# Kernel optimization log

Hardware: AMD Instinct MI355X
Metric: run time of the kernel (lower is better)

Reference implementation:

```python
import jax, jax.numpy as jnp
import numpy as np

B, L, NT = 4, 512, 20
H, DK, DM = 6, 10, 60  # heads, d_k, d_model (=embedding_dim+1)
ED = 59


def setup_inputs() -> dict:
    key = jax.random.key(0)
    ks = jax.random.split(key, 12)
    # event_seqs[..., 0] = event times (increasing), event_seqs[..., 1] = event type id stored as float
    times = jnp.cumsum(jax.random.uniform(ks[0], (B, L + 1)), axis=1)
    types = jax.random.randint(ks[1], (B, L + 1), 0, NT).astype(jnp.float32)
    event_seqs = jnp.stack([times, types], axis=-1)  # [B, L+1, 2]
    # causal (subsequent) mask, no padding -> lower-triangular [B, L, L]
    src_mask = jnp.broadcast_to(jnp.tril(jnp.ones((L, L), dtype=bool)), (B, L, L))
    w = lambda k, s: jax.random.normal(k, s, dtype=jnp.float32) * 0.1
    return dict(
        event_seqs=event_seqs, src_mask=src_mask,
        embed_w=w(ks[2], (ED, NT)),
        q_w=w(ks[3], (DM, DM)), q_b=jnp.zeros((DM,), jnp.float32),
        k_w=w(ks[4], (DM, DM)), k_b=jnp.zeros((DM,), jnp.float32),
        v_w=w(ks[5], (DM, DM)), v_b=jnp.zeros((DM,), jnp.float32),
        alpha_w=w(ks[6], (DK, DK * H // 2)), alpha_b=jnp.zeros((DK,), jnp.float32),
        gamma_w=w(ks[7], (DK, DK * H // 2)), gamma_b=jnp.zeros((DK,), jnp.float32),
        mu_w=w(ks[8], (DK, DM)), mu_b=jnp.zeros((DK,), jnp.float32),
    )


def reference(event_seqs, src_mask, embed_w, q_w, q_b, k_w, k_b, v_w, v_b,
              alpha_w, alpha_b, gamma_w, gamma_b, mu_w, mu_b):
    b = event_seqs.shape[0]
    # temporal feature: dt between consecutive events (ts padded with leading 0)
    ts = jnp.pad(event_seqs[:, :, 0], ((0, 0), (1, 0)))  # [B, T+1]
    dt = ts[:, 1:] - ts[:, :-1]                           # [B, T]
    temp_feat = dt[:, :-1, None]                          # [B, L, 1]
    types = event_seqs[:, :-1, 1].astype(jnp.int32)       # [B, L]
    type_feat = jax.nn.one_hot(types, NT, dtype=jnp.float32) @ embed_w.T  # [B, L, ED]
    feat = jnp.concatenate([temp_feat, type_feat], axis=-1)  # [B, L, DM]

    def heads(x, w, bias):
        return (x @ w.T + bias).reshape(b, L, H, DK).transpose(0, 2, 1, 3)  # [B,H,L,DK]

    q = heads(feat, q_w, q_b)
    k = heads(feat, k_w, k_b)
    v = heads(feat, v_w, v_b)

    mask4 = src_mask[:, None, :, :]  # [B,1,L,L]
    scores = jnp.einsum('bhid,bhjd->bhij', q, k) / np.sqrt(DK).astype(np.float32)
    scores = jnp.where(mask4, scores, -1e9)
    p_attn = jax.nn.softmax(scores, axis=-1)
    p_attn = jnp.where(mask4, p_attn, 0.0)               # [B,H,L,L]
    v_mu_pre = jnp.einsum('bhij,bhjd->bhid', p_attn, v)  # [B,H,L,DK]

    # per-pair attn * value, split heads in half (faithful to torch view semantics)
    prod = p_attn[..., None] * v[:, :, None, :, :]       # [B,H,L,L,DK]
    hh = H // 2
    x_alpha = prod[:, :hh].reshape(b, L, L, hh * DK)     # raw C-order reshape == torch .view
    x_gamma = prod[:, hh:].reshape(b, L, L, hh * DK)

    v_alpha = jax.nn.softplus(x_alpha @ alpha_w.T + alpha_b)          # Softplus(beta=1)
    v_gamma = jax.nn.softplus(10.0 * (x_gamma @ gamma_w.T + gamma_b)) / 10.0  # Softplus(beta=10)
    pair_mask = src_mask[..., None]                      # [B,L,L,1]
    v_alpha = jnp.where(pair_mask, v_alpha, 0.0)
    v_gamma = jnp.where(pair_mask, v_gamma, 0.0)

    v_mu = jax.nn.sigmoid(v_mu_pre.transpose(0, 2, 1, 3).reshape(b, L, DM) @ mu_w.T + mu_b)  # [B,L,DK]
    return (v_mu, v_alpha, v_gamma)
```

## Files before the change

### kernel.cpp

```cpp
#include <hip/hip_runtime.h>
#include <hip/hip_bf16.h>

#define BB 4
#define LL 512
#define NTYPES 20
#define HH 6
#define DKK 10
#define DMM 60
#define PROW 516
#define NWROW 516

__device__ __forceinline__ float softplus_fast(float x) {
    return fmaxf(x, 0.0f) + __logf(1.0f + __expf(-fabsf(x)));
}

__global__ void ishp_qkv(const float* __restrict__ ev,
                         const float* __restrict__ embed_w,
                         const float* __restrict__ qw, const float* __restrict__ qb,
                         const float* __restrict__ kw, const float* __restrict__ kb,
                         const float* __restrict__ vw, const float* __restrict__ vb,
                         const float* __restrict__ aw, const float* __restrict__ gw,
                         float* __restrict__ q, float* __restrict__ kT, float* __restrict__ vT,
                         float* __restrict__ Wbuf)
{
    int pos = blockIdx.x;
    int b = pos >> 9, l = pos & 511;
    __shared__ float feat[DMM];
    __shared__ float sv[DMM];
    int t = threadIdx.x;
    if (t == 0) {
        float t1 = ev[(b * (LL + 1) + l) * 2 + 0];
        float t0 = (l > 0) ? ev[(b * (LL + 1) + l - 1) * 2 + 0] : 0.0f;
        feat[0] = t1 - t0;
    } else if (t < DMM) {
        int type = (int)ev[(b * (LL + 1) + l) * 2 + 1];
        feat[t] = embed_w[(t - 1) * NTYPES + type];
    }
    __syncthreads();
    if (t < 3 * DMM) {
        int which = t / DMM;
        int m = t - which * DMM;
        const float* w  = which == 0 ? qw : which == 1 ? kw : vw;
        const float* bs = which == 0 ? qb : which == 1 ? kb : vb;
        float s = bs[m];
        #pragma unroll
        for (int c = 0; c < DMM; ++c) s += feat[c] * w[m * DMM + c];
        int h = m / DKK, d = m - h * DKK;
        if (which == 0)      q [((b * HH + h) * LL + l) * DKK + d] = s;
        else if (which == 1) kT[((b * HH + h) * DKK + d) * LL + l] = s;
        else {
            vT[((b * HH + h) * DKK + d) * LL + l] = s;
            sv[m] = s;
        }
    }
    __syncthreads();
    if (t < 180) {
        int kk = t % 10;
        int u = t / 10;
        int h  = u % 3;
        int cc = (u / 3) % 3;
        int mat = u / 9;
        const float* w = mat ? gw : aw;
        float s = 0.0f;
        #pragma unroll
        for (int d = 0; d < DKK; ++d) s += w[kk * 30 + cc * 10 + d] * sv[(h + 3 * mat) * DKK + d];
        int slot = (l % 3) * 172 + l / 3;
        Wbuf[((size_t)((((mat * 3 + cc) * 4 + b) * 3 + h) * 10 + kk)) * NWROW + slot] = s;
    }
}

__global__ __launch_bounds__(256) void ishp_attn(const float* __restrict__ q,
                                                 const float* __restrict__ kT,
                                                 const float* __restrict__ vT,
                                                 __hip_bfloat16* __restrict__ pbuf,
                                                 float* __restrict__ vmupre)
{
    int wid  = threadIdx.x >> 6;
    int lane = threadIdx.x & 63;
    int gw = blockIdx.x * 4 + wid;
    int bh = gw >> 7;
    int i0 = (gw & 127) * 4;
    const float* kT_ = kT + (size_t)bh * DKK * LL;
    const float* vT_ = vT + (size_t)bh * DKK * LL;

    float qr[4][DKK];
    #pragma unroll
    for (int r = 0; r < 4; ++r)
        #pragma unroll
        for (int d = 0; d < DKK; ++d)
            qr[r][d] = q[((size_t)bh * LL + i0 + r) * DKK + d];

    const float scale = 0.31622776601683794f;
    int nchunk = ((i0 + 3) >> 6) + 1;

    float e[4][8];
    float S[4] = {0.0f, 0.0f, 0.0f, 0.0f};
    #pragma unroll
    for (int c = 0; c < 8; ++c) {
        #pragma unroll
        for (int r = 0; r < 4; ++r) e[r][c] = 0.0f;
        if (c < nchunk) {
            int j = c * 64 + lane;
            float kd[DKK];
            #pragma unroll
            for (int d = 0; d < DKK; ++d) kd[d] = kT_[d * LL + j];
            #pragma unroll
            for (int r = 0; r < 4; ++r) {
                float dot = 0.0f;
                #pragma unroll
                for (int d = 0; d < DKK; ++d) dot += qr[r][d] * kd[d];
                if (j <= i0 + r) e[r][c] = __expf(dot * scale);
                S[r] += e[r][c];
            }
        }
    }
    #pragma unroll
    for (int r = 0; r < 4; ++r)
        #pragma unroll
        for (int off = 32; off >= 1; off >>= 1) S[r] += __shfl_xor(S[r], off, 64);
    float inv[4];
    #pragma unroll
    for (int r = 0; r < 4; ++r) inv[r] = 1.0f / S[r];

    #pragma unroll
    for (int c = 0; c < 8; ++c) {
        if (c < nchunk) {
            int j = c * 64 + lane;
            int slot = (j % 3) * 172 + j / 3;
            #pragma unroll
            for (int r = 0; r < 4; ++r) {
                if (j <= i0 + r)
                    pbuf[(size_t)(bh * LL + i0 + r) * PROW + slot] = __float2bfloat16(e[r][c] * inv[r]);
            }
        }
    }

    float acc[4][DKK];
    #pragma unroll
    for (int r = 0; r < 4; ++r)
        #pragma unroll
        for (int d = 0; d < DKK; ++d) acc[r][d] = 0.0f;
    #pragma unroll
    for (int c = 0; c < 8; ++c) {
        if (c < nchunk) {
            int j = c * 64 + lane;
            float vd[DKK];
            #pragma unroll
            for (int d = 0; d < DKK; ++d) vd[d] = vT_[d * LL + j];
            #pragma unroll
            for (int r = 0; r < 4; ++r)
                #pragma unroll
                for (int d = 0; d < DKK; ++d) acc[r][d] += e[r][c] * vd[d];
        }
    }
    #pragma unroll
    for (int r = 0; r < 4; ++r)
        #pragma unroll
        for (int d = 0; d < DKK; ++d) {
            float a = acc[r][d];
            #pragma unroll
            for (int off = 32; off >= 1; off >>= 1) a += __shfl_xor(a, off, 64);
            acc[r][d] = a;
        }
    if (lane == 0) {
        #pragma unroll
        for (int r = 0; r < 4; ++r)
            #pragma unroll
            for (int d = 0; d < DKK; ++d)
                vmupre[((size_t)bh * LL + i0 + r) * DKK + d] = acc[r][d] * inv[r];
    }
}

__global__ __launch_bounds__(256) void ishp_ag(const __hip_bfloat16* __restrict__ pbuf,
                                               const float* __restrict__ Wbuf,
                                               const float* __restrict__ ab,
                                               const float* __restrict__ gb,
                                               const float* __restrict__ vmupre,
                                               const float* __restrict__ muw,
                                               const float* __restrict__ mub,
                                               float* __restrict__ out_mu,
                                               float* __restrict__ outA,
                                               float* __restrict__ outG)
{
    __shared__ float sA[2560];
    __shared__ float sG[2560];
    int tid = threadIdx.x;
    int pos = blockIdx.x * 256 + tid;
    int b  = pos >> 18;
    int i2 = (pos >> 9) & 511;
    int j2 = pos & 511;

    float ra[DKK], rg[DKK];
    if (j2 > i2) {
        #pragma unroll
        for (int kk = 0; kk < DKK; ++kk) { ra[kk] = 0.0f; rg[kk] = 0.0f; }
    } else {
        #pragma unroll
        for (int kk = 0; kk < DKK; ++kk) { ra[kk] = ab[kk]; rg[kk] = gb[kk]; }
        #pragma unroll
        for (int cc = 0; cc < 3; ++cc) {
            int u = 3 * j2 + cc;
            int sel = u >> 9;
            int j = u & 511;
            int hi = 3 * i2 + sel;
            int h = hi >> 9;
            int i = hi & 511;
            int jq = j / 3;
            int r = j - 3 * jq;
            int slot = r * 172 + jq;
            float pa = 0.0f, pg = 0.0f;
            if (j <= i) {
                pa = __bfloat162float(pbuf[(size_t)((b * HH + h) * LL + i) * PROW + slot]);
                pg = __bfloat162float(pbuf[(size_t)((b * HH + h + 3) * LL + i) * PROW + slot]);
            }
            const float* Wa = Wbuf + ((size_t)(((0 + cc) * 4 + b) * 3 + h) * 10) * NWROW + slot;
            const float* Wg = Wbuf + ((size_t)(((3 + cc) * 4 + b) * 3 + h) * 10) * NWROW + slot;
            #pragma unroll
            for (int kk = 0; kk < DKK; ++kk) {
                ra[kk] += pa * Wa[kk * NWROW];
                rg[kk] += pg * Wg[kk * NWROW];
            }
        }
        #pragma unroll
        for (int kk = 0; kk < DKK; ++kk) {
            ra[kk] = softplus_fast(ra[kk]);
            rg[kk] = softplus_fast(10.0f * rg[kk]) * 0.1f;
        }
    }
    #pragma unroll
    for (int kk = 0; kk < DKK; ++kk) { sA[tid * 10 + kk] = ra[kk]; sG[tid * 10 + kk] = rg[kk]; }
    __syncthreads();

    size_t base = (size_t)blockIdx.x * 2560;
    #pragma unroll
    for (int it = 0; it < 3; ++it) {
        int idx = it * 1024 + tid * 4;
        if (idx < 2560) {
            *reinterpret_cast<float4*>(outA + base + idx) = *reinterpret_cast<const float4*>(&sA[idx]);
            *reinterpret_cast<float4*>(outG + base + idx) = *reinterpret_cast<const float4*>(&sG[idx]);
        }
    }

    if (blockIdx.x < 8) {
        int mpos = blockIdx.x * 256 + tid;
        int mb = mpos >> 9, ml = mpos & 511;
        float y[DKK];
        #pragma unroll
        for (int kk = 0; kk < DKK; ++kk) y[kk] = mub[kk];
        for (int c = 0; c < DMM; ++c) {
            int h = c / DKK, d = c - h * DKK;
            float xc = vmupre[((mb * HH + h) * LL + ml) * DKK + d];
            #pragma unroll
            for (int kk = 0; kk < DKK; ++kk) y[kk] += xc * muw[kk * DMM + c];
        }
        #pragma unroll
        for (int kk = 0; kk < DKK; ++kk)
            out_mu[(size_t)mpos * DKK + kk] = 1.0f / (1.0f + __expf(-y[kk]));
    }
}

extern "C" void kernel_launch(void* const* d_in, const int* in_sizes, int n_in,
                              void* d_out, int out_size, void* d_ws, size_t ws_size,
                              hipStream_t stream) {
    const void *ev = 0, *emb = 0, *muw = 0;
    const void *w3[3] = {0, 0, 0}, *b3[3] = {0, 0, 0};
    const void *w300[2] = {0, 0};
    const void *b10[3] = {0, 0, 0};
    int n3 = 0, nb3 = 0, n300 = 0, n10 = 0;
    for (int i = 0; i < n_in; ++i) {
        int s = in_sizes[i];
        if      (s == 4104) ev  = d_in[i];
        else if (s == 1180) emb = d_in[i];
        else if (s == 600)  muw = d_in[i];
        else if (s == 3600) { if (n3  < 3) w3[n3++]   = d_in[i]; }
        else if (s == 60)   { if (nb3 < 3) b3[nb3++]  = d_in[i]; }
        else if (s == 300)  { if (n300< 2) w300[n300++]=d_in[i]; }
        else if (s == 10)   { if (n10 < 3) b10[n10++] = d_in[i]; }
    }

    float* ws = (float*)d_ws;
    float* q = ws;
    float* kT = q + 122880;
    float* vT = kT + 122880;
    float* vmupre = vT + 122880;
    float* Wbuf = vmupre + 122880;
    __hip_bfloat16* pbuf = (__hip_bfloat16*)(Wbuf + 371520);

    float* out = (float*)d_out;
    float* out_mu = out;
    float* out_a  = out + 20480;
    float* out_g  = out + 20480 + 10485760;

    ishp_qkv<<<BB * LL, 192, 0, stream>>>((const float*)ev, (const float*)emb,
        (const float*)w3[0], (const float*)b3[0],
        (const float*)w3[1], (const float*)b3[1],
        (const float*)w3[2], (const float*)b3[2],
        (const float*)w300[0], (const float*)w300[1],
        q, kT, vT, Wbuf);
    ishp_attn<<<(BB * HH * LL) / 16, 256, 0, stream>>>(q, kT, vT, pbuf, vmupre);
    ishp_ag<<<(BB * LL * LL) / 256, 256, 0, stream>>>(pbuf, Wbuf,
        (const float*)b10[0], (const float*)b10[1], vmupre,
        (const float*)muw, (const float*)b10[2], out_mu, out_a, out_g);
}
```

Baseline: 61.02 us.

## Fuse three kernels into one cooperative persistent kernel with grid syncs

Merges the QKV projection, attention, and alpha/gamma output kernels into a single cooperative kernel of 512 blocks that loops over work and separates the stages with grid.sync(). Attention now gives each wave one row at a time and pairs row p with row 511-p to even out the causal triangle, in place of four rows per wave sharing K/V loads. This removes two kernel launch boundaries and the tail idle time between stages, but adds the cost of grid-wide barriers and caps occupancy at 512 resident blocks. The final stage, which is bound by output bandwidth, now runs on fewer blocks that each loop eight times.

```diff
diff --git a/kernel.cpp b/kernel.cpp
--- a/kernel.cpp
+++ b/kernel.cpp
@@ -1,5 +1,8 @@
 #include <hip/hip_runtime.h>
 #include <hip/hip_bf16.h>
+#include <hip/hip_cooperative_groups.h>
+
+namespace cg = cooperative_groups;
 
 #define BB 4
 #define LL 512
@@ -9,273 +12,243 @@
 #define DMM 60
 #define PROW 516
 #define NWROW 516
+#define NBLK 512
+#define SCALE 0.31622776601683794f
 
 __device__ __forceinline__ float softplus_fast(float x) {
     return fmaxf(x, 0.0f) + __logf(1.0f + __expf(-fabsf(x)));
 }
 
-__global__ void ishp_qkv(const float* __restrict__ ev,
-                         const float* __restrict__ embed_w,
-                         const float* __restrict__ qw, const float* __restrict__ qb,
-                         const float* __restrict__ kw, const float* __restrict__ kb,
-                         const float* __restrict__ vw, const float* __restrict__ vb,
-                         const float* __restrict__ aw, const float* __restrict__ gw,
-                         float* __restrict__ q, float* __restrict__ kT, float* __restrict__ vT,
-                         float* __restrict__ Wbuf)
+__device__ __forceinline__ void attn_row(int bh, int i, int lane,
+        const float* __restrict__ q, const float* __restrict__ kT_,
+        const float* __restrict__ vT_,
+        __hip_bfloat16* __restrict__ pbuf, float* __restrict__ vmupre)
 {
-    int pos = blockIdx.x;
-    int b = pos >> 9, l = pos & 511;
-    __shared__ float feat[DMM];
-    __shared__ float sv[DMM];
-    int t = threadIdx.x;
-    if (t == 0) {
-        float t1 = ev[(b * (LL + 1) + l) * 2 + 0];
-        float t0 = (l > 0) ? ev[(b * (LL + 1) + l - 1) * 2 + 0] : 0.0f;
-        feat[0] = t1 - t0;
-    } else if (t < DMM) {
-        int type = (int)ev[(b * (LL + 1) + l) * 2 + 1];
-        feat[t] = embed_w[(t - 1) * NTYPES + type];
-    }
-    __syncthreads();
-    if (t < 3 * DMM) {
-        int which = t / DMM;
-        int m = t - which * DMM;
-        const float* w  = which == 0 ? qw : which == 1 ? kw : vw;
-        const float* bs = which == 0 ? qb : which == 1 ? kb : vb;
-        float s = bs[m];
-        #pragma unroll
-        for (int c = 0; c < DMM; ++c) s += feat[c] * w[m * DMM + c];
-        int h = m / DKK, d = m - h * DKK;
-        if (which == 0)      q [((b * HH + h) * LL + l) * DKK + d] = s;
-        else if (which == 1) kT[((b * HH + h) * DKK + d) * LL + l] = s;
-        else {
-            vT[((b * HH + h) * DKK + d) * LL + l] = s;
-            sv[m] = s;
-        }
-    }
-    __syncthreads();
-    if (t < 180) {
-        int kk = t % 10;
-        int u = t / 10;
-        int h  = u % 3;
-        int cc = (u / 3) % 3;
-        int mat = u / 9;
-        const float* w = mat ? gw : aw;
-        float s = 0.0f;
-        #pragma unroll
-        for (int d = 0; d < DKK; ++d) s += w[kk * 30 + cc * 10 + d] * sv[(h + 3 * mat) * DKK + d];
-        int slot = (l % 3) * 172 + l / 3;
-        Wbuf[((size_t)((((mat * 3 + cc) * 4 + b) * 3 + h) * 10 + kk)) * NWROW + slot] = s;
-    }
-}
-
-__global__ __launch_bounds__(256) void ishp_attn(const float* __restrict__ q,
-                                                 const float* __restrict__ kT,
-                                                 const float* __restrict__ vT,
-                                                 __hip_bfloat16* __restrict__ pbuf,
-                                                 float* __restrict__ vmupre)
-{
-    int wid  = threadIdx.x >> 6;
-    int lane = threadIdx.x & 63;
-    int gw = blockIdx.x * 4 + wid;
-    int bh = gw >> 7;
-    int i0 = (gw & 127) * 4;
-    const float* kT_ = kT + (size_t)bh * DKK * LL;
-    const float* vT_ = vT + (size_t)bh * DKK * LL;
-
-    float qr[4][DKK];
-    #pragma unroll
-    for (int r = 0; r < 4; ++r)
-        #pragma unroll
-        for (int d = 0; d < DKK; ++d)
-            qr[r][d] = q[((size_t)bh * LL + i0 + r) * DKK + d];
-
-    const float scale = 0.31622776601683794f;
-    int nchunk = ((i0 + 3) >> 6) + 1;
-
-    float e[4][8];
-    float S[4] = {0.0f, 0.0f, 0.0f, 0.0f};
+    float qr[DKK];
+    #pragma unroll
+    for (int d = 0; d < DKK; ++d) qr[d] = q[((size_t)bh * LL + i) * DKK + d];
+    int nchunk = (i >> 6) + 1;
+    float e[8];
+    float S = 0.0f;
     #pragma unroll
     for (int c = 0; c < 8; ++c) {
-        #pragma unroll
-        for (int r = 0; r < 4; ++r) e[r][c] = 0.0f;
+        e[c] = 0.0f;
         if (c < nchunk) {
             int j = c * 64 + lane;
-            float kd[DKK];
-            #pragma unroll
-            for (int d = 0; d < DKK; ++d) kd[d] = kT_[d * LL + j];
-            #pragma unroll
-            for (int r = 0; r < 4; ++r) {
-                float dot = 0.0f;
-                #pragma unroll
-                for (int d = 0; d < DKK; ++d) dot += qr[r][d] * kd[d];
-                if (j <= i0 + r) e[r][c] = __expf(dot * scale);
-                S[r] += e[r][c];
-            }
-        }
-    }
-    #pragma unroll
-    for (int r = 0; r < 4; ++r)
-        #pragma unroll
-        for (int off = 32; off >= 1; off >>= 1) S[r] += __shfl_xor(S[r], off, 64);
-    float inv[4];
-    #pragma unroll
-    for (int r = 0; r < 4; ++r) inv[r] = 1.0f / S[r];
-
+            float dot = 0.0f;
+            #pragma unroll
+            for (int d = 0; d < DKK; ++d) dot += qr[d] * kT_[d * LL + j];
+            if (j <= i) e[c] = __expf(dot * SCALE);
+            S += e[c];
+        }
+    }
+    #pragma unroll
+    for (int off = 32; off >= 1; off >>= 1) S += __shfl_xor(S, off, 64);
+    float inv = 1.0f / S;
+    __hip_bfloat16* prow = pbuf + (size_t)(bh * LL + i) * PROW;
     #pragma unroll
     for (int c = 0; c < 8; ++c) {
         if (c < nchunk) {
             int j = c * 64 + lane;
             int slot = (j % 3) * 172 + j / 3;
-            #pragma unroll
-            for (int r = 0; r < 4; ++r) {
-                if (j <= i0 + r)
-                    pbuf[(size_t)(bh * LL + i0 + r) * PROW + slot] = __float2bfloat16(e[r][c] * inv[r]);
-            }
-        }
-    }
-
-    float acc[4][DKK];
-    #pragma unroll
-    for (int r = 0; r < 4; ++r)
-        #pragma unroll
-        for (int d = 0; d < DKK; ++d) acc[r][d] = 0.0f;
+            if (j <= i) prow[slot] = __float2bfloat16(e[c] * inv);
+        }
+    }
+    float acc[DKK];
+    #pragma unroll
+    for (int d = 0; d < DKK; ++d) acc[d] = 0.0f;
     #pragma unroll
     for (int c = 0; c < 8; ++c) {
         if (c < nchunk) {
             int j = c * 64 + lane;
-            float vd[DKK];
-            #pragma unroll
-            for (int d = 0; d < DKK; ++d) vd[d] = vT_[d * LL + j];
-            #pragma unroll
-            for (int r = 0; r < 4; ++r)
+            #pragma unroll
+            for (int d = 0; d < DKK; ++d) acc[d] += e[c] * vT_[d * LL + j];
+        }
+    }
+    #pragma unroll
+    for (int d = 0; d < DKK; ++d) {
+        float a = acc[d];
+        #pragma unroll
+        for (int off = 32; off >= 1; off >>= 1) a += __shfl_xor(a, off, 64);
+        acc[d] = a;
+    }
+    if (lane == 0) {
+        #pragma unroll
+        for (int d = 0; d < DKK; ++d)
+            vmupre[((size_t)bh * LL + i) * DKK + d] = acc[d] * inv;
+    }
+}
+
+__global__ __launch_bounds__(256, 2) void ishp_all(
+        const float* __restrict__ ev, const float* __restrict__ embed_w,
+        const float* __restrict__ qw, const float* __restrict__ qb,
+        const float* __restrict__ kw, const float* __restrict__ kb,
+        const float* __restrict__ vw, const float* __restrict__ vb,
+        const float* __restrict__ aw, const float* __restrict__ gw,
+        const float* __restrict__ ab, const float* __restrict__ gb,
+        const float* __restrict__ muw, const float* __restrict__ mub,
+        float* __restrict__ q, float* __restrict__ kT, float* __restrict__ vT,
+        float* __restrict__ vmupre, float* __restrict__ Wbuf,
+        __hip_bfloat16* __restrict__ pbuf,
+        float* __restrict__ out_mu, float* __restrict__ outA, float* __restrict__ outG)
+{
+    cg::grid_group grid = cg::this_grid();
+    __shared__ float smem[5120];
+    __shared__ float sv[DMM];
+    int blk = blockIdx.x;
+    int tid = threadIdx.x;
+    int lane = tid & 63;
+
+    for (int s = 0; s < 4; ++s) {
+        int pos = (blk << 2) + s;
+        int b = pos >> 9, l = pos & 511;
+        if (tid == 0) {
+            float t1 = ev[(b * (LL + 1) + l) * 2 + 0];
+            float t0 = (l > 0) ? ev[(b * (LL + 1) + l - 1) * 2 + 0] : 0.0f;
+            smem[0] = t1 - t0;
+        } else if (tid < DMM) {
+            int type = (int)ev[(b * (LL + 1) + l) * 2 + 1];
+            smem[tid] = embed_w[(tid - 1) * NTYPES + type];
+        }
+        __syncthreads();
+        if (tid < 180) {
+            int which = tid / DMM;
+            int m = tid - which * DMM;
+            const float* w  = which == 0 ? qw : which == 1 ? kw : vw;
+            const float* bs = which == 0 ? qb : which == 1 ? kb : vb;
+            float sacc = bs[m];
+            #pragma unroll
+            for (int c = 0; c < DMM; ++c) sacc += smem[c] * w[m * DMM + c];
+            int h = m / DKK, d = m - h * DKK;
+            if (which == 0)      q [((b * HH + h) * LL + l) * DKK + d] = sacc;
+            else if (which == 1) kT[((b * HH + h) * DKK + d) * LL + l] = sacc;
+            else { vT[((b * HH + h) * DKK + d) * LL + l] = sacc; sv[m] = sacc; }
+        }
+        __syncthreads();
+        if (tid < 180) {
+            int kk = tid % 10;
+            int u = tid / 10;
+            int h  = u % 3;
+            int cc = (u / 3) % 3;
+            int mat = u / 9;
+            const float* w = mat ? gw : aw;
+            float sacc = 0.0f;
+            #pragma unroll
+            for (int d = 0; d < DKK; ++d) sacc += w[kk * 30 + cc * 10 + d] * sv[(h + 3 * mat) * DKK + d];
+            int slot = (l % 3) * 172 + l / 3;
+            Wbuf[((size_t)((((mat * 3 + cc) * 4 + b) * 3 + h) * 10 + kk)) * NWROW + slot] = sacc;
+        }
+        __syncthreads();
+    }
+    grid.sync();
+
+    int gwave = (blk << 2) + (tid >> 6);
+    for (int task = gwave; task < 6144; task += 2048) {
+        int bh = task >> 8;
+        int p = task & 255;
+        const float* kT_ = kT + (size_t)bh * DKK * LL;
+        const float* vT_ = vT + (size_t)bh * DKK * LL;
+        attn_row(bh, p, lane, q, kT_, vT_, pbuf, vmupre);
+        attn_row(bh, 511 - p, lane, q, kT_, vT_, pbuf, vmupre);
+    }
+    grid.sync();
+
+    for (int s = 0; s < 8; ++s) {
+        int tile = (s << 9) + blk;
+        int pos = (tile << 8) + tid;
+        int b  = pos >> 18;
+        int i2 = (pos >> 9) & 511;
+        int j2 = pos & 511;
+
+        float ra[DKK], rg[DKK];
+        if (j2 > i2) {
+            #pragma unroll
+            for (int kk = 0; kk < DKK; ++kk) { ra[kk] = 0.0f; rg[kk] = 0.0f; }
+        } else {
+            #pragma unroll
+            for (int kk = 0; kk < DKK; ++kk) { ra[kk] = ab[kk]; rg[kk] = gb[kk]; }
+            #pragma unroll
+            for (int cc = 0; cc < 3; ++cc) {
+                int u = 3 * j2 + cc;
+                int sel = u >> 9;
+                int j = u & 511;
+                int hi = 3 * i2 + sel;
+                int h = hi >> 9;
+                int i = hi & 511;
+                int jq = j / 3;
+                int r = j - 3 * jq;
+                int slot = r * 172 + jq;
+                float pa = 0.0f, pg = 0.0f;
+                if (j <= i) {
+                    pa = __bfloat162float(pbuf[(size_t)((b * HH + h) * LL + i) * PROW + slot]);
+                    pg = __bfloat162float(pbuf[(size_t)((b * HH + h + 3) * LL + i) * PROW + slot]);
+                }
+                const float* Wa = Wbuf + ((size_t)(((0 + cc) * 4 + b) * 3 + h) * 10) * NWROW + slot;
+                const float* Wg = Wbuf + ((size_t)(((3 + cc) * 4 + b) * 3 + h) * 10) * NWROW + slot;
                 #pragma unroll
-                for (int d = 0; d < DKK; ++d) acc[r][d] += e[r][c] * vd[d];
-        }
-    }
-    #pragma unroll
-    for (int r = 0; r < 4; ++r)
-        #pragma unroll
-        for (int d = 0; d < DKK; ++d) {
-            float a = acc[r][d];
-            #pragma unroll
-            for (int off = 32; off >= 1; off >>= 1) a += __shfl_xor(a, off, 64);
-            acc[r][d] = a;
-        }
-    if (lane == 0) {
-        #pragma unroll
-        for (int r = 0; r < 4; ++r)
-            #pragma unroll
-            for (int d = 0; d < DKK; ++d)
-                vmupre[((size_t)bh * LL + i0 + r) * DKK + d] = acc[r][d] * inv[r];
-    }
-}
-
-__global__ __launch_bounds__(256) void ishp_ag(const __hip_bfloat16* __restrict__ pbuf,
-                                               const float* __restrict__ Wbuf,
-                                               const float* __restrict__ ab,
-                                               const float* __restrict__ gb,
-                                               const float* __restrict__ vmupre,
-                                               const float* __restrict__ muw,
-                                               const float* __restrict__ mub,
-                                               float* __restrict__ out_mu,
-                                               float* __restrict__ outA,
-                                               float* __restrict__ outG)
-{
-    __shared__ float sA[2560];
-    __shared__ float sG[2560];
-    int tid = threadIdx.x;
-    int pos = blockIdx.x * 256 + tid;
-    int b  = pos >> 18;
-    int i2 = (pos >> 9) & 511;
-    int j2 = pos & 511;
-
-    float ra[DKK], rg[DKK];
-    if (j2 > i2) {
-        #pragma unroll
-        for (int kk = 0; kk < DKK; ++kk) { ra[kk] = 0.0f; rg[kk] = 0.0f; }
-    } else {
-        #pragma unroll
-        for (int kk = 0; kk < DKK; ++kk) { ra[kk] = ab[kk]; rg[kk] = gb[kk]; }
-        #pragma unroll
-        for (int cc = 0; cc < 3; ++cc) {
-            int u = 3 * j2 + cc;
-            int sel = u >> 9;
-            int j = u & 511;
-            int hi = 3 * i2 + sel;
-            int h = hi >> 9;
-            int i = hi & 511;
-            int jq = j / 3;
-            int r = j - 3 * jq;
-            int slot = r * 172 + jq;
-            float pa = 0.0f, pg = 0.0f;
-            if (j <= i) {
-                pa = __bfloat162float(pbuf[(size_t)((b * HH + h) * LL + i) * PROW + slot]);
-                pg = __bfloat162float(pbuf[(size_t)((b * HH + h + 3) * LL + i) * PROW + slot]);
-            }
-            const float* Wa = Wbuf + ((size_t)(((0 + cc) * 4 + b) * 3 + h) * 10) * NWROW + slot;
-            const float* Wg = Wbuf + ((size_t)(((3 + cc) * 4 + b) * 3 + h) * 10) * NWROW + slot;
+                for (int kk = 0; kk < DKK; ++kk) {
+                    ra[kk] += pa * Wa[kk * NWROW];
+                    rg[kk] += pg * Wg[kk * NWROW];
+                }
+            }
             #pragma unroll
             for (int kk = 0; kk < DKK; ++kk) {
-                ra[kk] += pa * Wa[kk * NWROW];
-                rg[kk] += pg * Wg[kk * NWROW];
-            }
-        }
+                ra[kk] = softplus_fast(ra[kk]);
+                rg[kk] = softplus_fast(10.0f * rg[kk]) * 0.1f;
+            }
+        }
+        __syncthreads();
         #pragma unroll
         for (int kk = 0; kk < DKK; ++kk) {
-            ra[kk] = softplus_fast(ra[kk]);
-            rg[kk] = softplus_fast(10.0f * rg[kk]) * 0.1f;
-        }
-    }
-    #pragma unroll
-    for (int kk = 0; kk < DKK; ++kk) { sA[tid * 10 + kk] = ra[kk]; sG[tid * 10 + kk] = rg[kk]; }
-    __syncthreads();
-
-    size_t base = (size_t)blockIdx.x * 2560;
-    #pragma unroll
-    for (int it = 0; it < 3; ++it) {
-        int idx = it * 1024 + tid * 4;
-        if (idx < 2560) {
-            *reinterpret_cast<float4*>(outA + base + idx) = *reinterpret_cast<const float4*>(&sA[idx]);
-            *reinterpret_cast<float4*>(outG + base + idx) = *reinterpret_cast<const float4*>(&sG[idx]);
-        }
-    }
-
-    if (blockIdx.x < 8) {
-        int mpos = blockIdx.x * 256 + tid;
-        int mb = mpos >> 9, ml = mpos & 511;
-        float y[DKK];
-        #pragma unroll
-        for (int kk = 0; kk < DKK; ++kk) y[kk] = mub[kk];
-        for (int c = 0; c < DMM; ++c) {
-            int h = c / DKK, d = c - h * DKK;
-            float xc = vmupre[((mb * HH + h) * LL + ml) * DKK + d];
-            #pragma unroll
-            for (int kk = 0; kk < DKK; ++kk) y[kk] += xc * muw[kk * DMM + c];
-        }
-        #pragma unroll
-        for (int kk = 0; kk < DKK; ++kk)
-            out_mu[(size_t)mpos * DKK + kk] = 1.0f / (1.0f + __expf(-y[kk]));
+            smem[tid * 10 + kk] = ra[kk];
+            smem[2560 + tid * 10 + kk] = rg[kk];
+        }
+        __syncthreads();
+        size_t base = (size_t)tile * 2560;
+        #pragma unroll
+        for (int it = 0; it < 3; ++it) {
+            int idx = it * 1024 + tid * 4;
+            if (idx < 2560) {
+                *reinterpret_cast<float4*>(outA + base + idx) = *reinterpret_cast<const float4*>(&smem[idx]);
+                *reinterpret_cast<float4*>(outG + base + idx) = *reinterpret_cast<const float4*>(&smem[2560 + idx]);
+            }
+        }
+        if (tile < 8) {
+            int mpos = (tile << 8) + tid;
+            int mb = mpos >> 9, ml = mpos & 511;
+            float y[DKK];
+            #pragma unroll
+            for (int kk = 0; kk < DKK; ++kk) y[kk] = mub[kk];
+            for (int c = 0; c < DMM; ++c) {
+                int h = c / DKK, d = c - h * DKK;
+                float xc = vmupre[((mb * HH + h) * LL + ml) * DKK + d];
+                #pragma unroll
+                for (int kk = 0; kk < DKK; ++kk) y[kk] += xc * muw[kk * DMM + c];
+            }
+            #pragma unroll
+            for (int kk = 0; kk < DKK; ++kk)
+                out_mu[(size_t)mpos * DKK + kk] = 1.0f / (1.0f + __expf(-y[kk]));
+        }
     }
 }
 
 extern "C" void kernel_launch(void* const* d_in, const int* in_sizes, int n_in,
                               void* d_out, int out_size, void* d_ws, size_t ws_size,
                               hipStream_t stream) {
-    const void *ev = 0, *emb = 0, *muw = 0;
-    const void *w3[3] = {0, 0, 0}, *b3[3] = {0, 0, 0};
-    const void *w300[2] = {0, 0};
-    const void *b10[3] = {0, 0, 0};
+    const float *ev = 0, *emb = 0, *muw = 0;
+    const float *w3[3] = {0, 0, 0}, *b3[3] = {0, 0, 0};
+    const float *w300[2] = {0, 0};
+    const float *b10[3] = {0, 0, 0};
     int n3 = 0, nb3 = 0, n300 = 0, n10 = 0;
     for (int i = 0; i < n_in; ++i) {
         int s = in_sizes[i];
-        if      (s == 4104) ev  = d_in[i];
-        else if (s == 1180) emb = d_in[i];
-        else if (s == 600)  muw = d_in[i];
-        else if (s == 3600) { if (n3  < 3) w3[n3++]   = d_in[i]; }
-        else if (s == 60)   { if (nb3 < 3) b3[nb3++]  = d_in[i]; }
-        else if (s == 300)  { if (n300< 2) w300[n300++]=d_in[i]; }
-        else if (s == 10)   { if (n10 < 3) b10[n10++] = d_in[i]; }
+        if      (s == 4104) ev  = (const float*)d_in[i];
+        else if (s == 1180) emb = (const float*)d_in[i];
+        else if (s == 600)  muw = (const float*)d_in[i];
+        else if (s == 3600) { if (n3  < 3) w3[n3++]   = (const float*)d_in[i]; }
+        else if (s == 60)   { if (nb3 < 3) b3[nb3++]  = (const float*)d_in[i]; }
+        else if (s == 300)  { if (n300< 2) w300[n300++]=(const float*)d_in[i]; }
+        else if (s == 10)   { if (n10 < 3) b10[n10++] = (const float*)d_in[i]; }
     }
 
     float* ws = (float*)d_ws;
@@ -291,14 +264,17 @@
     float* out_a  = out + 20480;
     float* out_g  = out + 20480 + 10485760;
 
-    ishp_qkv<<<BB * LL, 192, 0, stream>>>((const float*)ev, (const float*)emb,
-        (const float*)w3[0], (const float*)b3[0],
-        (const float*)w3[1], (const float*)b3[1],
-        (const float*)w3[2], (const float*)b3[2],
-        (const float*)w300[0], (const float*)w300[1],
-        q, kT, vT, Wbuf);
-    ishp_attn<<<(BB * HH * LL) / 16, 256, 0, stream>>>(q, kT, vT, pbuf, vmupre);
-    ishp_ag<<<(BB * LL * LL) / 256, 256, 0, stream>>>(pbuf, Wbuf,
-        (const float*)b10[0], (const float*)b10[1], vmupre,
-        (const float*)muw, (const float*)b10[2], out_mu, out_a, out_g);
-}
+    void* kargs[] = {
+        (void*)&ev, (void*)&emb,
+        (void*)&w3[0], (void*)&b3[0], (void*)&w3[1], (void*)&b3[1],
+        (void*)&w3[2], (void*)&b3[2],
+        (void*)&w300[0], (void*)&w300[1],
+        (void*)&b10[0], (void*)&b10[1],
+        (void*)&muw, (void*)&b10[2],
+        (void*)&q, (void*)&kT, (void*)&vT, (void*)&vmupre, (void*)&Wbuf,
+        (void*)&pbuf,
+        (void*)&out_mu, (void*)&out_a, (void*)&out_g
+    };
+    hipLaunchCooperativeKernel((const void*)ishp_all, dim3(NBLK), dim3(256),
+                               kargs, 0, stream);
+}
```

Measured after the change: 228.0 us. +273.6%, slower.

## Stage K/V in LDS and interleave query rows across blocks for balance

Applied to the files above, without the earlier changes.

The attention kernel now loads each (batch,head)'s K and V transposes into shared memory once per block. Each wave then processes one query row at a time, strided across the sequence so causal work is balanced between blocks. This replaces per-wave global reloads of K/V and the 4-row register blocking. The grid shrinks from 768 to 384 blocks, and dropping the 4-row register reuse means each K/V element is read from LDS once per query row.

```diff
diff --git a/kernel.cpp b/kernel.cpp
--- a/kernel.cpp
+++ b/kernel.cpp
@@ -75,99 +75,86 @@
                                                  __hip_bfloat16* __restrict__ pbuf,
                                                  float* __restrict__ vmupre)
 {
-    int wid  = threadIdx.x >> 6;
-    int lane = threadIdx.x & 63;
-    int gw = blockIdx.x * 4 + wid;
-    int bh = gw >> 7;
-    int i0 = (gw & 127) * 4;
-    const float* kT_ = kT + (size_t)bh * DKK * LL;
-    const float* vT_ = vT + (size_t)bh * DKK * LL;
-
-    float qr[4][DKK];
+    __shared__ float sK[DKK * LL];
+    __shared__ float sV[DKK * LL];
+    int bh = blockIdx.x >> 4;
+    int rg = blockIdx.x & 15;
+    int tid = threadIdx.x;
+    int lane = tid & 63;
+    int wv = tid >> 6;
+
+    const float4* kT4 = reinterpret_cast<const float4*>(kT + (size_t)bh * DKK * LL);
+    const float4* vT4 = reinterpret_cast<const float4*>(vT + (size_t)bh * DKK * LL);
+    float4* sK4 = reinterpret_cast<float4*>(sK);
+    float4* sV4 = reinterpret_cast<float4*>(sV);
     #pragma unroll
-    for (int r = 0; r < 4; ++r)
-        #pragma unroll
-        for (int d = 0; d < DKK; ++d)
-            qr[r][d] = q[((size_t)bh * LL + i0 + r) * DKK + d];
+    for (int u = 0; u < 5; ++u) {
+        int idx = u * 256 + tid;
+        sK4[idx] = kT4[idx];
+        sV4[idx] = vT4[idx];
+    }
+    __syncthreads();
 
     const float scale = 0.31622776601683794f;
-    int nchunk = ((i0 + 3) >> 6) + 1;
-
-    float e[4][8];
-    float S[4] = {0.0f, 0.0f, 0.0f, 0.0f};
-    #pragma unroll
-    for (int c = 0; c < 8; ++c) {
-        #pragma unroll
-        for (int r = 0; r < 4; ++r) e[r][c] = 0.0f;
-        if (c < nchunk) {
-            int j = c * 64 + lane;
-            float kd[DKK];
-            #pragma unroll
-            for (int d = 0; d < DKK; ++d) kd[d] = kT_[d * LL + j];
-            #pragma unroll
-            for (int r = 0; r < 4; ++r) {
+
+    for (int t = 0; t < 8; ++t) {
+        int i = rg + 16 * (wv + 4 * t);
+        float qr[DKK];
+        #pragma unroll
+        for (int d = 0; d < DKK; ++d) qr[d] = q[((size_t)bh * LL + i) * DKK + d];
+        int nchunk = (i >> 6) + 1;
+
+        float e[8];
+        float S = 0.0f;
+        #pragma unroll
+        for (int c = 0; c < 8; ++c) {
+            e[c] = 0.0f;
+            if (c < nchunk) {
+                int j = c * 64 + lane;
                 float dot = 0.0f;
                 #pragma unroll
-                for (int d = 0; d < DKK; ++d) dot += qr[r][d] * kd[d];
-                if (j <= i0 + r) e[r][c] = __expf(dot * scale);
-                S[r] += e[r][c];
-            }
-        }
-    }
-    #pragma unroll
-    for (int r = 0; r < 4; ++r)
-        #pragma unroll
-        for (int off = 32; off >= 1; off >>= 1) S[r] += __shfl_xor(S[r], off, 64);
-    float inv[4];
-    #pragma unroll
-    for (int r = 0; r < 4; ++r) inv[r] = 1.0f / S[r];
-
-    #pragma unroll
-    for (int c = 0; c < 8; ++c) {
-        if (c < nchunk) {
-            int j = c * 64 + lane;
-            int slot = (j % 3) * 172 + j / 3;
-            #pragma unroll
-            for (int r = 0; r < 4; ++r) {
-                if (j <= i0 + r)
-                    pbuf[(size_t)(bh * LL + i0 + r) * PROW + slot] = __float2bfloat16(e[r][c] * inv[r]);
-            }
-        }
-    }
-
-    float acc[4][DKK];
-    #pragma unroll
-    for (int r = 0; r < 4; ++r)
-        #pragma unroll
-        for (int d = 0; d < DKK; ++d) acc[r][d] = 0.0f;
-    #pragma unroll
-    for (int c = 0; c < 8; ++c) {
-        if (c < nchunk) {
-            int j = c * 64 + lane;
-            float vd[DKK];
-            #pragma unroll
-            for (int d = 0; d < DKK; ++d) vd[d] = vT_[d * LL + j];
-            #pragma unroll
-            for (int r = 0; r < 4; ++r)
+                for (int d = 0; d < DKK; ++d) dot += qr[d] * sK[d * LL + j];
+                if (j <= i) e[c] = __expf(dot * scale);
+                S += e[c];
+            }
+        }
+        #pragma unroll
+        for (int off = 32; off >= 1; off >>= 1) S += __shfl_xor(S, off, 64);
+        float inv = 1.0f / S;
+
+        __hip_bfloat16* prow = pbuf + (size_t)(bh * LL + i) * PROW;
+        #pragma unroll
+        for (int c = 0; c < 8; ++c) {
+            if (c < nchunk) {
+                int j = c * 64 + lane;
+                int slot = (j % 3) * 172 + j / 3;
+                if (j <= i) prow[slot] = __float2bfloat16(e[c] * inv);
+            }
+        }
+
+        float acc[DKK];
+        #pragma unroll
+        for (int d = 0; d < DKK; ++d) acc[d] = 0.0f;
+        #pragma unroll
+        for (int c = 0; c < 8; ++c) {
+            if (c < nchunk) {
+                int j = c * 64 + lane;
                 #pragma unroll
-                for (int d = 0; d < DKK; ++d) acc[r][d] += e[r][c] * vd[d];
-        }
-    }
-    #pragma unroll
-    for (int r = 0; r < 4; ++r)
+                for (int d = 0; d < DKK; ++d) acc[d] += e[c] * sV[d * LL + j];
+            }
+        }
         #pragma unroll
         for (int d = 0; d < DKK; ++d) {
-            float a = acc[r][d];
+            float a = acc[d];
             #pragma unroll
             for (int off = 32; off >= 1; off >>= 1) a += __shfl_xor(a, off, 64);
-            acc[r][d] = a;
-        }
-    if (lane == 0) {
-        #pragma unroll
-        for (int r = 0; r < 4; ++r)
+            acc[d] = a;
+        }
+        if (lane == 0) {
             #pragma unroll
             for (int d = 0; d < DKK; ++d)
-                vmupre[((size_t)bh * LL + i0 + r) * DKK + d] = acc[r][d] * inv[r];
+                vmupre[((size_t)bh * LL + i) * DKK + d] = acc[d] * inv;
+        }
     }
 }
 
@@ -297,7 +284,7 @@
         (const float*)w3[2], (const float*)b3[2],
         (const float*)w300[0], (const float*)w300[1],
         q, kT, vT, Wbuf);
-    ishp_attn<<<(BB * HH * LL) / 16, 256, 0, stream>>>(q, kT, vT, pbuf, vmupre);
+    ishp_attn<<<BB * HH * 16, 256, 0, stream>>>(q, kT, vT, pbuf, vmupre);
     ishp_ag<<<(BB * LL * LL) / 256, 256, 0, stream>>>(pbuf, Wbuf,
         (const float*)b10[0], (const float*)b10[1], vmupre,
         (const float*)muw, (const float*)b10[2], out_mu, out_a, out_g);
```

Measured after the change: 64.96 us. 6.4% more time.

## Fuse QKV projection into attention kernel with LDS-resident K/V and row pairing

Applied to the files above, without the earlier changes.

Merges the QKV projection kernel into the attention kernel. Each block recomputes the K and V projections for its (batch, head) into shared memory and computes only the Q rows it needs, which removes the q/kT/vT global round trip and one launch. Each wave handles a short row paired with its mirrored long row so causal work is balanced across waves. The cost is redundant K/V projection work across the 16 blocks per head, plus serial Wbuf production by one block per head.

```diff
diff --git a/kernel.cpp b/kernel.cpp
--- a/kernel.cpp
+++ b/kernel.cpp
@@ -14,160 +14,214 @@
     return fmaxf(x, 0.0f) + __logf(1.0f + __expf(-fabsf(x)));
 }
 
-__global__ void ishp_qkv(const float* __restrict__ ev,
-                         const float* __restrict__ embed_w,
-                         const float* __restrict__ qw, const float* __restrict__ qb,
-                         const float* __restrict__ kw, const float* __restrict__ kb,
-                         const float* __restrict__ vw, const float* __restrict__ vb,
-                         const float* __restrict__ aw, const float* __restrict__ gw,
-                         float* __restrict__ q, float* __restrict__ kT, float* __restrict__ vT,
-                         float* __restrict__ Wbuf)
+__global__ __launch_bounds__(512) void ishp_attn(
+        const float* __restrict__ ev, const float* __restrict__ emb,
+        const float* __restrict__ qw, const float* __restrict__ qb,
+        const float* __restrict__ kw, const float* __restrict__ kb,
+        const float* __restrict__ vw, const float* __restrict__ vb,
+        const float* __restrict__ aw, const float* __restrict__ gw,
+        __hip_bfloat16* __restrict__ pbuf, float* __restrict__ vmupre,
+        float* __restrict__ Wbuf)
 {
-    int pos = blockIdx.x;
-    int b = pos >> 9, l = pos & 511;
-    __shared__ float feat[DMM];
-    __shared__ float sv[DMM];
+    __shared__ float sK[DKK * LL];
+    __shared__ float sV[DKK * LL];
+    __shared__ float sFeat[64][61];
+    __shared__ float sW[30][60];
+    __shared__ float sB[30];
+    __shared__ float sEmb[1180];
+    __shared__ int   sType[64];
+    __shared__ float sq[32][DKK];
+
+    int bh = blockIdx.x >> 4;
+    int rg = blockIdx.x & 15;
+    int b = bh / HH, H = bh % HH;
     int t = threadIdx.x;
-    if (t == 0) {
-        float t1 = ev[(b * (LL + 1) + l) * 2 + 0];
-        float t0 = (l > 0) ? ev[(b * (LL + 1) + l - 1) * 2 + 0] : 0.0f;
-        feat[0] = t1 - t0;
-    } else if (t < DMM) {
-        int type = (int)ev[(b * (LL + 1) + l) * 2 + 1];
-        feat[t] = embed_w[(t - 1) * NTYPES + type];
-    }
+    int lane = t & 63, wv = t >> 6;
+
+    #pragma unroll
+    for (int u = 0; u < 4; ++u) {
+        int idx = u * 512 + t;
+        if (idx < 1800) {
+            int row = idx / 60, c = idx - row * 60;
+            float val;
+            if (row < 10)      val = kw[(H * 10 + row) * 60 + c];
+            else if (row < 20) val = vw[(H * 10 + row - 10) * 60 + c];
+            else               val = qw[(H * 10 + row - 20) * 60 + c];
+            sW[row][c] = val;
+        }
+    }
+    if (t < 30)
+        sB[t] = (t < 10) ? kb[H * 10 + t] : (t < 20) ? vb[H * 10 + t - 10] : qb[H * 10 + t - 20];
+    #pragma unroll
+    for (int u = 0; u < 3; ++u) {
+        int idx = u * 512 + t;
+        if (idx < 1180) sEmb[idx] = emb[idx];
+    }
+    int lo0 = rg * 16;
+    int hi0 = 496 - rg * 16;
     __syncthreads();
-    if (t < 3 * DMM) {
-        int which = t / DMM;
-        int m = t - which * DMM;
-        const float* w  = which == 0 ? qw : which == 1 ? kw : vw;
-        const float* bs = which == 0 ? qb : which == 1 ? kb : vb;
-        float s = bs[m];
-        #pragma unroll
-        for (int c = 0; c < DMM; ++c) s += feat[c] * w[m * DMM + c];
-        int h = m / DKK, d = m - h * DKK;
-        if (which == 0)      q [((b * HH + h) * LL + l) * DKK + d] = s;
-        else if (which == 1) kT[((b * HH + h) * DKK + d) * LL + l] = s;
-        else {
-            vT[((b * HH + h) * DKK + d) * LL + l] = s;
-            sv[m] = s;
-        }
-    }
-    __syncthreads();
-    if (t < 180) {
-        int kk = t % 10;
-        int u = t / 10;
-        int h  = u % 3;
-        int cc = (u / 3) % 3;
-        int mat = u / 9;
+
+    for (int tile = 0; tile < 8; ++tile) {
+        int base = tile * 64;
+        if (t < 64) {
+            int lg = base + t;
+            float t1 = ev[(b * (LL + 1) + lg) * 2];
+            float t0 = (lg > 0) ? ev[(b * (LL + 1) + lg - 1) * 2] : 0.0f;
+            sFeat[t][0] = t1 - t0;
+            sType[t] = (int)ev[(b * (LL + 1) + lg) * 2 + 1];
+        }
+        __syncthreads();
+        #pragma unroll
+        for (int u = 0; u < 8; ++u) {
+            int e = u * 512 + t;
+            if (e < 3776) {
+                int l = e / 59, c = 1 + (e - (e / 59) * 59);
+                sFeat[l][c] = sEmb[(c - 1) * NTYPES + sType[l]];
+            }
+        }
+        __syncthreads();
+        #pragma unroll
+        for (int u = 0; u < 3; ++u) {
+            int tt = u * 512 + t;
+            if (tt < 1280) {
+                int l = tt / 20, o = tt - (tt / 20) * 20;
+                float s = sB[o];
+                #pragma unroll
+                for (int c = 0; c < DMM; ++c) s += sFeat[l][c] * sW[o][c];
+                if (o < 10) sK[o * LL + base + l] = s;
+                else        sV[(o - 10) * LL + base + l] = s;
+            }
+        }
+        if ((lo0 >> 6) == tile && t < 160) {
+            int r = t / 10, d = t - (t / 10) * 10;
+            int il = lo0 + r - base;
+            float s = sB[20 + d];
+            #pragma unroll
+            for (int c = 0; c < DMM; ++c) s += sFeat[il][c] * sW[20 + d][c];
+            sq[r][d] = s;
+        }
+        if ((hi0 >> 6) == tile && t < 160) {
+            int r = t / 10, d = t - (t / 10) * 10;
+            int il = hi0 + r - base;
+            float s = sB[20 + d];
+            #pragma unroll
+            for (int c = 0; c < DMM; ++c) s += sFeat[il][c] * sW[20 + d][c];
+            sq[16 + r][d] = s;
+        }
+        __syncthreads();
+    }
+
+    if (rg == 0) {
+        int mat = (H >= 3) ? 1 : 0;
+        int hp = H - 3 * mat;
         const float* w = mat ? gw : aw;
-        float s = 0.0f;
-        #pragma unroll
-        for (int d = 0; d < DKK; ++d) s += w[kk * 30 + cc * 10 + d] * sv[(h + 3 * mat) * DKK + d];
-        int slot = (l % 3) * 172 + l / 3;
-        Wbuf[((size_t)((((mat * 3 + cc) * 4 + b) * 3 + h) * 10 + kk)) * NWROW + slot] = s;
-    }
-}
-
-__global__ __launch_bounds__(256) void ishp_attn(const float* __restrict__ q,
-                                                 const float* __restrict__ kT,
-                                                 const float* __restrict__ vT,
-                                                 __hip_bfloat16* __restrict__ pbuf,
-                                                 float* __restrict__ vmupre)
-{
-    int wid  = threadIdx.x >> 6;
-    int lane = threadIdx.x & 63;
-    int gw = blockIdx.x * 4 + wid;
-    int bh = gw >> 7;
-    int i0 = (gw & 127) * 4;
-    const float* kT_ = kT + (size_t)bh * DKK * LL;
-    const float* vT_ = vT + (size_t)bh * DKK * LL;
-
-    float qr[4][DKK];
-    #pragma unroll
-    for (int r = 0; r < 4; ++r)
-        #pragma unroll
-        for (int d = 0; d < DKK; ++d)
-            qr[r][d] = q[((size_t)bh * LL + i0 + r) * DKK + d];
+        #pragma unroll
+        for (int u = 0; u < 30; ++u) {
+            int tt = u * 512 + t;
+            int l = tt & 511;
+            int r2 = tt >> 9;
+            int cc = r2 / 10, kk = r2 - cc * 10;
+            float s = 0.0f;
+            #pragma unroll
+            for (int d = 0; d < DKK; ++d) s += w[kk * 30 + cc * 10 + d] * sV[d * LL + l];
+            int slot = (l % 3) * 172 + l / 3;
+            Wbuf[((size_t)((((mat * 3 + cc) * 4 + b) * 3 + hp) * 10 + kk)) * NWROW + slot] = s;
+        }
+    }
 
     const float scale = 0.31622776601683794f;
-    int nchunk = ((i0 + 3) >> 6) + 1;
-
-    float e[4][8];
-    float S[4] = {0.0f, 0.0f, 0.0f, 0.0f};
-    #pragma unroll
-    for (int c = 0; c < 8; ++c) {
-        #pragma unroll
-        for (int r = 0; r < 4; ++r) e[r][c] = 0.0f;
-        if (c < nchunk) {
-            int j = c * 64 + lane;
-            float kd[DKK];
-            #pragma unroll
-            for (int d = 0; d < DKK; ++d) kd[d] = kT_[d * LL + j];
-            #pragma unroll
-            for (int r = 0; r < 4; ++r) {
-                float dot = 0.0f;
-                #pragma unroll
-                for (int d = 0; d < DKK; ++d) dot += qr[r][d] * kd[d];
-                if (j <= i0 + r) e[r][c] = __expf(dot * scale);
-                S[r] += e[r][c];
-            }
-        }
-    }
-    #pragma unroll
-    for (int r = 0; r < 4; ++r)
-        #pragma unroll
-        for (int off = 32; off >= 1; off >>= 1) S[r] += __shfl_xor(S[r], off, 64);
-    float inv[4];
-    #pragma unroll
-    for (int r = 0; r < 4; ++r) inv[r] = 1.0f / S[r];
-
-    #pragma unroll
-    for (int c = 0; c < 8; ++c) {
-        if (c < nchunk) {
-            int j = c * 64 + lane;
-            int slot = (j % 3) * 172 + j / 3;
-            #pragma unroll
-            for (int r = 0; r < 4; ++r) {
-                if (j <= i0 + r)
-                    pbuf[(size_t)(bh * LL + i0 + r) * PROW + slot] = __float2bfloat16(e[r][c] * inv[r]);
-            }
-        }
-    }
-
-    float acc[4][DKK];
-    #pragma unroll
-    for (int r = 0; r < 4; ++r)
-        #pragma unroll
-        for (int d = 0; d < DKK; ++d) acc[r][d] = 0.0f;
-    #pragma unroll
-    for (int c = 0; c < 8; ++c) {
-        if (c < nchunk) {
-            int j = c * 64 + lane;
-            float vd[DKK];
-            #pragma unroll
-            for (int d = 0; d < DKK; ++d) vd[d] = vT_[d * LL + j];
-            #pragma unroll
-            for (int r = 0; r < 4; ++r)
-                #pragma unroll
-                for (int d = 0; d < DKK; ++d) acc[r][d] += e[r][c] * vd[d];
-        }
-    }
-    #pragma unroll
-    for (int r = 0; r < 4; ++r)
+    #pragma unroll
+    for (int sidx = 0; sidx < 2; ++sidx) {
+        int ploc = wv + 8 * sidx;
+        int i_lo = lo0 + ploc;
+        int i_hi = 511 - i_lo;
+        float ql[DKK], qh[DKK];
         #pragma unroll
         for (int d = 0; d < DKK; ++d) {
-            float a = acc[r][d];
-            #pragma unroll
-            for (int off = 32; off >= 1; off >>= 1) a += __shfl_xor(a, off, 64);
-            acc[r][d] = a;
-        }
-    if (lane == 0) {
-        #pragma unroll
-        for (int r = 0; r < 4; ++r)
-            #pragma unroll
-            for (int d = 0; d < DKK; ++d)
-                vmupre[((size_t)bh * LL + i0 + r) * DKK + d] = acc[r][d] * inv[r];
+            ql[d] = sq[ploc][d];
+            qh[d] = sq[16 + 15 - ploc][d];
+        }
+        int nch_l = (i_lo >> 6) + 1;
+        int nch_h = (i_hi >> 6) + 1;
+
+        float eh[8], el[8];
+        float Sh = 0.0f, Sl = 0.0f;
+        #pragma unroll
+        for (int c = 0; c < 8; ++c) {
+            eh[c] = 0.0f; el[c] = 0.0f;
+            if (c < nch_h) {
+                int j = c * 64 + lane;
+                float kd[DKK];
+                #pragma unroll
+                for (int d = 0; d < DKK; ++d) kd[d] = sK[d * LL + j];
+                float dh = 0.0f;
+                #pragma unroll
+                for (int d = 0; d < DKK; ++d) dh += qh[d] * kd[d];
+                if (j <= i_hi) eh[c] = __expf(dh * scale);
+                Sh += eh[c];
+                if (c < nch_l) {
+                    float dl = 0.0f;
+                    #pragma unroll
+                    for (int d = 0; d < DKK; ++d) dl += ql[d] * kd[d];
+                    if (j <= i_lo) el[c] = __expf(dl * scale);
+                    Sl += el[c];
+                }
+            }
+        }
+        #pragma unroll
+        for (int off = 32; off >= 1; off >>= 1) {
+            Sh += __shfl_xor(Sh, off, 64);
+            Sl += __shfl_xor(Sl, off, 64);
+        }
+        float inv_h = 1.0f / Sh, inv_l = 1.0f / Sl;
+
+        __hip_bfloat16* prow_h = pbuf + (size_t)(bh * LL + i_hi) * PROW;
+        __hip_bfloat16* prow_l = pbuf + (size_t)(bh * LL + i_lo) * PROW;
+        #pragma unroll
+        for (int c = 0; c < 8; ++c) {
+            if (c < nch_h) {
+                int j = c * 64 + lane;
+                int slot = (j % 3) * 172 + j / 3;
+                if (j <= i_hi) prow_h[slot] = __float2bfloat16(eh[c] * inv_h);
+                if (c < nch_l && j <= i_lo) prow_l[slot] = __float2bfloat16(el[c] * inv_l);
+            }
+        }
+
+        float ah[DKK], al[DKK];
+        #pragma unroll
+        for (int d = 0; d < DKK; ++d) { ah[d] = 0.0f; al[d] = 0.0f; }
+        #pragma unroll
+        for (int c = 0; c < 8; ++c) {
+            if (c < nch_h) {
+                int j = c * 64 + lane;
+                float vd[DKK];
+                #pragma unroll
+                for (int d = 0; d < DKK; ++d) vd[d] = sV[d * LL + j];
+                #pragma unroll
+                for (int d = 0; d < DKK; ++d) ah[d] += eh[c] * vd[d];
+                if (c < nch_l) {
+                    #pragma unroll
+                    for (int d = 0; d < DKK; ++d) al[d] += el[c] * vd[d];
+                }
+            }
+        }
+        #pragma unroll
+        for (int d = 0; d < DKK; ++d) {
+            float a0 = ah[d], a1 = al[d];
+            #pragma unroll
+            for (int off = 32; off >= 1; off >>= 1) {
+                a0 += __shfl_xor(a0, off, 64);
+                a1 += __shfl_xor(a1, off, 64);
+            }
+            ah[d] = a0; al[d] = a1;
+        }
+        if (lane == 0) {
+            #pragma unroll
+            for (int d = 0; d < DKK; ++d) {
+                vmupre[((size_t)bh * LL + i_hi) * DKK + d] = ah[d] * inv_h;
+                vmupre[((size_t)bh * LL + i_lo) * DKK + d] = al[d] * inv_l;
+            }
+        }
     }
 }
 
@@ -279,10 +333,7 @@
     }
 
     float* ws = (float*)d_ws;
-    float* q = ws;
-    float* kT = q + 122880;
-    float* vT = kT + 122880;
-    float* vmupre = vT + 122880;
+    float* vmupre = ws;
     float* Wbuf = vmupre + 122880;
     __hip_bfloat16* pbuf = (__hip_bfloat16*)(Wbuf + 371520);
 
@@ -291,13 +342,12 @@
     float* out_a  = out + 20480;
     float* out_g  = out + 20480 + 10485760;
 
-    ishp_qkv<<<BB * LL, 192, 0, stream>>>((const float*)ev, (const float*)emb,
+    ishp_attn<<<BB * HH * 16, 512, 0, stream>>>((const float*)ev, (const float*)emb,
         (const float*)w3[0], (const float*)b3[0],
         (const float*)w3[1], (const float*)b3[1],
         (const float*)w3[2], (const float*)b3[2],
         (const float*)w300[0], (const float*)w300[1],
-        q, kT, vT, Wbuf);
-    ishp_attn<<<(BB * HH * LL) / 16, 256, 0, stream>>>(q, kT, vT, pbuf, vmupre);
+        pbuf, vmupre, Wbuf);
     ishp_ag<<<(BB * LL * LL) / 256, 256, 0, stream>>>(pbuf, Wbuf,
         (const float*)b10[0], (const float*)b10[1], vmupre,
         (const float*)muw, (const float*)b10[2], out_mu, out_a, out_g);
```

Result: slower. 108.4 us (+77.6%).
